# Kernel tuning notes

Measured on AMD Instinct MI355X. Metric: run time of the kernel, lower is better.

The kernel has to match this reference:

```python
import jax, jax.numpy as jnp
import numpy as np

B, H, W, DIM = 64, 28, 28, 384
N = B * H * W
E, K, R = 3, 2, 8
HID = 4 * DIM
SCALING = 8.0 / 8.0  # alpha / r


def setup_inputs() -> dict:
    key = jax.random.key(0)
    ks = jax.random.split(key, 8)
    x = jax.random.normal(ks[0], (B, H, W, DIM), dtype=jnp.float32)
    gate = jax.random.uniform(ks[1], (N, E), dtype=jnp.float32)
    topk_probs = jax.random.uniform(ks[2], (N, K), dtype=jnp.float32)
    topk_idx = jax.random.randint(ks[3], (N, K), 0, E)
    # LoRA expert params (w_up is zeros in the original init; use small randn
    # so the MoE path is numerically non-trivial for kernel testing)
    w_down = jax.random.normal(ks[4], (E, DIM, R), dtype=jnp.float32) * (1.0 / DIM ** 0.5)
    w_up = jax.random.normal(ks[5], (E, R, DIM), dtype=jnp.float32) * 0.02
    # frozen base ConvNeXt MLP: Linear(dim,4dim) -> GELU -> Linear(4dim,dim)
    W1 = jax.random.normal(ks[6], (DIM, HID), dtype=jnp.float32) * 0.02
    b1 = jnp.zeros((HID,), dtype=jnp.float32)
    W2 = jax.random.normal(ks[7], (HID, DIM), dtype=jnp.float32) * 0.02
    b2 = jnp.zeros((DIM,), dtype=jnp.float32)
    return {"x": x, "gate": gate, "topk_probs": topk_probs, "topk_idx": topk_idx,
            "w_down": w_down, "w_up": w_up, "W1": W1, "b1": b1, "W2": W2, "b2": b2}


def reference(x, gate, topk_probs, topk_idx, w_down, w_up, W1, b1, W2, b2):
    gelu = lambda t: jax.nn.gelu(t, approximate=False)  # torch nn.GELU() default = exact erf
    # frozen base MLP
    orig = gelu(jnp.einsum('bhwd,df->bhwf', x, W1) + b1)
    orig = jnp.einsum('bhwf,fd->bhwd', orig, W2) + b2
    # MoE LoRA path over flattened tokens
    x_flat = x.reshape(-1, x.shape[-1])          # [N, dim]
    moe = jnp.zeros_like(x_flat)
    n_experts = w_down.shape[0]
    for i in range(n_experts):
        # combined routing weight for expert i (0 for tokens not routed here)
        prob = jnp.sum(jnp.where(topk_idx == i, topk_probs, 0.0), axis=1)  # [N]
        out_i = gelu(x_flat @ w_down[i]) @ w_up[i] * SCALING               # [N, dim]
        moe = moe + out_i * prob[:, None]
    return orig + moe.reshape(x.shape)
```

## Files before the change

### kernel.cpp

```cpp
#include <hip/hip_runtime.h>
#include <hip/hip_bf16.h>

typedef __attribute__((ext_vector_type(4))) float float4v;
typedef __attribute__((ext_vector_type(8))) __bf16 bf16x8;
typedef __attribute__((ext_vector_type(8))) unsigned short ushort8v;

constexpr int NTOK = 50176;
constexpr int DIM  = 384;
constexpr int HID  = 1536;
constexpr int BM   = 64;
constexpr int NTH  = 512;
constexpr int NBLK = NTOK / BM;
constexpr int CHW  = 32;
constexpr int NCH  = HID / CHW;

constexpr int IMG_WD  = 0;
constexpr int IMG_WUP = 24576;
constexpr int IMG_W1  = 49152;
constexpr int IMG_W2  = 49152 + 48 * 12288 * 2;
constexpr size_t WS_NEED = 2408448;
constexpr int NELEMS = 1204224;

constexpr int L_X  = 0;
constexpr int L_W  = 49152;
constexpr int L_HS = 73728;
constexpr int LDSZ = 81920;

__device__ __forceinline__ unsigned short f2bf(float f) {
  __hip_bfloat16 h = __float2bfloat16(f);
  return *reinterpret_cast<unsigned short*>(&h);
}

__device__ __forceinline__ float gelu_f(float v) {
  float u = 0.7978845608f * (v + 0.044715f * v * v * v);
  float e = __expf(2.0f * u);
  float t = 1.0f - 2.0f / (e + 1.0f);
  return 0.5f * v * (1.0f + t);
}

__device__ __forceinline__ int gt_addr(int r, int s) {
  return ((r >> 3) << 9) + (s << 7) + ((r & 7) << 4);
}

__device__ __forceinline__ void st_load(const char* src, int tid, ushort8v st[3]) {
  #pragma unroll
  for (int j = 0; j < 3; ++j)
    st[j] = *(const ushort8v*)(src + tid * 16 + j * 8192);
}
__device__ __forceinline__ void st_wr(char* dst, int tid, const ushort8v st[3]) {
  #pragma unroll
  for (int j = 0; j < 3; ++j)
    *(ushort8v*)(dst + tid * 16 + j * 8192) = st[j];
}

__global__ __launch_bounds__(256) void pack_k(
    const float* __restrict__ W1, const float* __restrict__ W2,
    const float* __restrict__ wd, const float* __restrict__ wu,
    unsigned short* __restrict__ img)
{
  int i = blockIdx.x * 256 + threadIdx.x;
  if (i >= NELEMS) return;
  if (i < 12288) {
    int f = i / 384; int inb = (i % 384) * 2;
    int d = (inb ^ ((f & 7) << 4)) >> 1;
    float v = (f < 24) ? wd[(f >> 3) * (DIM * 8) + d * 8 + (f & 7)] : 0.f;
    img[i] = f2bf(v);
  } else if (i < 24576) {
    int j = i - 12288;
    int d = j / 32, c = j % 32;
    float v = (c < 24) ? wu[c * DIM + d] : 0.f;
    img[i] = f2bf(v);
  } else if (i < 24576 + 48 * 12288) {
    int j = i - 24576; int h = j / 12288; int jc = j % 12288;
    int f = jc / 384; int inb = (jc % 384) * 2;
    int d = (inb ^ ((f & 7) << 4)) >> 1;
    img[i] = f2bf(W1[d * HID + h * CHW + f]);
  } else {
    int j = i - 24576 - 48 * 12288; int h = j / 12288; int jc = j % 12288;
    int d = jc / 32, k = jc % 32;
    img[i] = f2bf(W2[(h * CHW + k) * DIM + d]);
  }
}

__global__ __launch_bounds__(NTH, 4) void fused_k(
    const float* __restrict__ x,
    const float* __restrict__ tp,
    const int*   __restrict__ ti,
    const float* __restrict__ b1,
    const float* __restrict__ b2,
    const unsigned short* __restrict__ img,
    float* __restrict__ out)
{
  extern __shared__ char lds[];
  const int tid = threadIdx.x, wid = tid >> 6, lane = tid & 63;
  const int lrow = lane & 15, g4 = lane >> 4;
  const int blockRow = blockIdx.x * BM;
  const char* imgc = (const char*)img;

  const int band = wid >> 1, chh = wid & 1;
  const int wr = wid >> 2, wc = wid & 3;

  ushort8v st[3];

  st_load(imgc + IMG_WD, tid, st);
  {
    const float* xb = x + (size_t)blockRow * DIM;
    #pragma unroll
    for (int it = 0; it < 6; ++it) {
      int idx = it * NTH + tid;
      int row = idx / 48, c8 = idx % 48;
      float4v v0 = *(const float4v*)(xb + row * DIM + c8 * 8);
      float4v v1 = *(const float4v*)(xb + row * DIM + c8 * 8 + 4);
      ushort8v u;
      u[0]=f2bf(v0[0]); u[1]=f2bf(v0[1]); u[2]=f2bf(v0[2]); u[3]=f2bf(v0[3]);
      u[4]=f2bf(v1[0]); u[5]=f2bf(v1[1]); u[6]=f2bf(v1[2]); u[7]=f2bf(v1[3]);
      int byte = (row * 768 + c8 * 16) ^ ((row & 7) << 4);
      *(ushort8v*)(lds + L_X + byte) = u;
    }
  }
  st_wr(lds + L_W, tid, st);
  st_load(imgc + IMG_W1, tid, st);
  __syncthreads();

  {
    float4v hv = {};
    int raX = band * 16 + lrow, sA = (raX & 7) << 4, baX = raX * 768 + g4 * 16;
    int rbW = chh * 16 + lrow, sB = (rbW & 7) << 4, baW = rbW * 768 + g4 * 16;
    #pragma unroll
    for (int ks = 0; ks < 12; ++ks) {
      bf16x8 a = *(const bf16x8*)(lds + L_X + ((baX + ks * 64) ^ sA));
      bf16x8 b = *(const bf16x8*)(lds + L_W + ((baW + ks * 64) ^ sB));
      hv = __builtin_amdgcn_mfma_f32_16x16x32_bf16(a, b, hv, 0, 0, 0);
    }
    int colc = chh * 16 + lrow; int e = colc >> 3;
    #pragma unroll
    for (int r = 0; r < 4; ++r) {
      int row = band * 16 + g4 * 4 + r;
      int token = blockRow + row;
      float p = 0.f;
      if (e < 3) {
        int i0 = ti[token * 2], i1 = ti[token * 2 + 1];
        if (i0 == e) p += tp[token * 2];
        if (i1 == e) p += tp[token * 2 + 1];
      }
      float gv = p * gelu_f(hv[r]);
      int byte = gt_addr(row, colc >> 3) + ((colc & 7) << 1);
      *(unsigned short*)(lds + L_HS + byte) = f2bf(gv);
    }
  }
  __syncthreads();
  st_wr(lds + L_W, tid, st);

  float4v acc[2][6] = {};
  {
    bf16x8 bfr[6];
    #pragma unroll
    for (int nt = 0; nt < 6; ++nt) {
      int rd = wc * 96 + nt * 16 + lrow;
      bfr[nt] = *(const bf16x8*)(imgc + IMG_WUP + rd * 64 + g4 * 16);
    }
    bf16x8 A[2];
    #pragma unroll
    for (int mt = 0; mt < 2; ++mt) {
      int ra = wr * 32 + mt * 16 + lrow;
      A[mt] = *(const bf16x8*)(lds + L_HS + gt_addr(ra, g4));
    }
    #pragma unroll
    for (int nt = 0; nt < 6; ++nt) {
      acc[0][nt] = __builtin_amdgcn_mfma_f32_16x16x32_bf16(A[0], bfr[nt], acc[0][nt], 0, 0, 0);
      acc[1][nt] = __builtin_amdgcn_mfma_f32_16x16x32_bf16(A[1], bfr[nt], acc[1][nt], 0, 0, 0);
    }
  }

  for (int h = 0; h < NCH; ++h) {
    const int hb = 4096 - ((h & 1) << 12);
    __syncthreads();
    if (h < NCH - 1)
      st_load(imgc + IMG_W1 + (h + 1) * 24576, tid, st);

    float4v hv = {};
    {
      int raX = band * 16 + lrow, sA = (raX & 7) << 4, baX = raX * 768 + g4 * 16;
      int rbW = chh * 16 + lrow, sB = (rbW & 7) << 4, baW = rbW * 768 + g4 * 16;
      #pragma unroll
      for (int ks = 0; ks < 12; ++ks) {
        bf16x8 a = *(const bf16x8*)(lds + L_X + ((baX + ks * 64) ^ sA));
        bf16x8 b = *(const bf16x8*)(lds + L_W + ((baW + ks * 64) ^ sB));
        hv = __builtin_amdgcn_mfma_f32_16x16x32_bf16(a, b, hv, 0, 0, 0);
      }
    }
    {
      int colc = chh * 16 + lrow;
      float bb = b1[h * CHW + colc];
      #pragma unroll
      for (int r = 0; r < 4; ++r) {
        int row = band * 16 + g4 * 4 + r;
        float gv = gelu_f(hv[r] + bb);
        int byte = gt_addr(row, colc >> 3) + ((colc & 7) << 1);
        *(unsigned short*)(lds + L_HS + hb + byte) = f2bf(gv);
      }
    }
    __syncthreads();
    if (h < NCH - 1)
      st_wr(lds + L_W, tid, st);

    {
      const char* w2b = imgc + IMG_W2 + h * 24576;
      bf16x8 bfr[6];
      #pragma unroll
      for (int nt = 0; nt < 6; ++nt) {
        int rd = wc * 96 + nt * 16 + lrow;
        bfr[nt] = *(const bf16x8*)(w2b + rd * 64 + g4 * 16);
      }
      bf16x8 A[2];
      #pragma unroll
      for (int mt = 0; mt < 2; ++mt) {
        int ra = wr * 32 + mt * 16 + lrow;
        A[mt] = *(const bf16x8*)(lds + L_HS + hb + gt_addr(ra, g4));
      }
      #pragma unroll
      for (int nt = 0; nt < 6; ++nt) {
        acc[0][nt] = __builtin_amdgcn_mfma_f32_16x16x32_bf16(A[0], bfr[nt], acc[0][nt], 0, 0, 0);
        acc[1][nt] = __builtin_amdgcn_mfma_f32_16x16x32_bf16(A[1], bfr[nt], acc[1][nt], 0, 0, 0);
      }
    }
  }

  #pragma unroll
  for (int nt = 0; nt < 6; ++nt) {
    int col = wc * 96 + nt * 16 + lrow;
    float bb = b2[col];
    #pragma unroll
    for (int mt = 0; mt < 2; ++mt) {
      #pragma unroll
      for (int r = 0; r < 4; ++r) {
        int row = wr * 32 + mt * 16 + g4 * 4 + r;
        out[(size_t)(blockRow + row) * DIM + col] = acc[mt][nt][r] + bb;
      }
    }
  }
}

extern "C" void kernel_launch(void* const* d_in, const int* in_sizes, int n_in,
                              void* d_out, int out_size, void* d_ws, size_t ws_size,
                              hipStream_t stream) {
  const float* x          = (const float*)d_in[0];
  const float* topk_probs = (const float*)d_in[2];
  const int*   topk_idx   = (const int*)  d_in[3];
  const float* w_down     = (const float*)d_in[4];
  const float* w_up       = (const float*)d_in[5];
  const float* W1         = (const float*)d_in[6];
  const float* b1         = (const float*)d_in[7];
  const float* W2         = (const float*)d_in[8];
  const float* b2         = (const float*)d_in[9];
  float* out = (float*)d_out;

  if (ws_size < WS_NEED) return;

  hipFuncSetAttribute(reinterpret_cast<const void*>(fused_k),
                      hipFuncAttributeMaxDynamicSharedMemorySize, LDSZ);

  unsigned short* img = (unsigned short*)d_ws;
  pack_k<<<(NELEMS + 255) / 256, 256, 0, stream>>>(W1, W2, w_down, w_up, img);
  fused_k<<<NBLK, NTH, LDSZ, stream>>>(x, topk_probs, topk_idx, b1, b2, img, out);
}
```

Measured before the change: 276.9 us.

## Give each wave its own 16-token strip with register-resident x and double-buffered W1

Reworks the fused MLP kernel so each of 4 waves owns 16 tokens. The bf16 x fragments stay in registers instead of LDS, and each wave computes all 32 hidden columns and all 384 output columns for its strip. W1 chunks are double-buffered in LDS, which removes one barrier per chunk. This cuts LDS traffic and synchronisation, at the cost of a 256-thread block, higher register pressure (24 accumulators plus 12 x fragments) and lower occupancy. Each wave also reads W2 fragments from global memory four times as often per chunk.

```diff
diff --git a/kernel.cpp b/kernel.cpp
--- a/kernel.cpp
+++ b/kernel.cpp
@@ -9,7 +9,7 @@
 constexpr int DIM  = 384;
 constexpr int HID  = 1536;
 constexpr int BM   = 64;
-constexpr int NTH  = 512;
+constexpr int NTH  = 256;
 constexpr int NBLK = NTOK / BM;
 constexpr int CHW  = 32;
 constexpr int NCH  = HID / CHW;
@@ -17,14 +17,12 @@
 constexpr int IMG_WD  = 0;
 constexpr int IMG_WUP = 24576;
 constexpr int IMG_W1  = 49152;
-constexpr int IMG_W2  = 49152 + 48 * 12288 * 2;
+constexpr int IMG_W2  = 49152 + 48 * 24576;
 constexpr size_t WS_NEED = 2408448;
 constexpr int NELEMS = 1204224;
 
-constexpr int L_X  = 0;
-constexpr int L_W  = 49152;
-constexpr int L_HS = 73728;
-constexpr int LDSZ = 81920;
+constexpr int L_HS = 49152;
+constexpr int LDSZ = 53248;
 
 __device__ __forceinline__ unsigned short f2bf(float f) {
   __hip_bfloat16 h = __float2bfloat16(f);
@@ -38,19 +36,26 @@
   return 0.5f * v * (1.0f + t);
 }
 
+__device__ __forceinline__ bf16x8 mk8(float4v a, float4v b) {
+  ushort8v u;
+  u[0]=f2bf(a[0]); u[1]=f2bf(a[1]); u[2]=f2bf(a[2]); u[3]=f2bf(a[3]);
+  u[4]=f2bf(b[0]); u[5]=f2bf(b[1]); u[6]=f2bf(b[2]); u[7]=f2bf(b[3]);
+  return *reinterpret_cast<bf16x8*>(&u);
+}
+
 __device__ __forceinline__ int gt_addr(int r, int s) {
   return ((r >> 3) << 9) + (s << 7) + ((r & 7) << 4);
 }
 
-__device__ __forceinline__ void st_load(const char* src, int tid, ushort8v st[3]) {
+__device__ __forceinline__ void stage_ld(const char* src, int tid, ushort8v t[6]) {
   #pragma unroll
-  for (int j = 0; j < 3; ++j)
-    st[j] = *(const ushort8v*)(src + tid * 16 + j * 8192);
-}
-__device__ __forceinline__ void st_wr(char* dst, int tid, const ushort8v st[3]) {
+  for (int j = 0; j < 6; ++j)
+    t[j] = *(const ushort8v*)(src + tid * 16 + j * 4096);
+}
+__device__ __forceinline__ void stage_wr(char* dst, int tid, const ushort8v t[6]) {
   #pragma unroll
-  for (int j = 0; j < 3; ++j)
-    *(ushort8v*)(dst + tid * 16 + j * 8192) = st[j];
+  for (int j = 0; j < 6; ++j)
+    *(ushort8v*)(dst + tid * 16 + j * 4096) = t[j];
 }
 
 __global__ __launch_bounds__(256) void pack_k(
@@ -82,7 +87,7 @@
   }
 }
 
-__global__ __launch_bounds__(NTH, 4) void fused_k(
+__global__ __launch_bounds__(NTH, 2) void fused_k(
     const float* __restrict__ x,
     const float* __restrict__ tp,
     const int*   __restrict__ ti,
@@ -95,148 +100,108 @@
   const int tid = threadIdx.x, wid = tid >> 6, lane = tid & 63;
   const int lrow = lane & 15, g4 = lane >> 4;
   const int blockRow = blockIdx.x * BM;
+  const int wtok = wid * 16;
   const char* imgc = (const char*)img;
-
-  const int band = wid >> 1, chh = wid & 1;
-  const int wr = wid >> 2, wc = wid & 3;
-
-  ushort8v st[3];
-
-  st_load(imgc + IMG_WD, tid, st);
+  const int swz = (lrow & 7) << 4;
+
+  ushort8v stg[6];
+
+  stage_ld(imgc + IMG_WD, tid, stg);
+  bf16x8 xf[12];
   {
-    const float* xb = x + (size_t)blockRow * DIM;
-    #pragma unroll
-    for (int it = 0; it < 6; ++it) {
-      int idx = it * NTH + tid;
-      int row = idx / 48, c8 = idx % 48;
-      float4v v0 = *(const float4v*)(xb + row * DIM + c8 * 8);
-      float4v v1 = *(const float4v*)(xb + row * DIM + c8 * 8 + 4);
-      ushort8v u;
-      u[0]=f2bf(v0[0]); u[1]=f2bf(v0[1]); u[2]=f2bf(v0[2]); u[3]=f2bf(v0[3]);
-      u[4]=f2bf(v1[0]); u[5]=f2bf(v1[1]); u[6]=f2bf(v1[2]); u[7]=f2bf(v1[3]);
-      int byte = (row * 768 + c8 * 16) ^ ((row & 7) << 4);
-      *(ushort8v*)(lds + L_X + byte) = u;
-    }
-  }
-  st_wr(lds + L_W, tid, st);
-  st_load(imgc + IMG_W1, tid, st);
+    const float* xr = x + (size_t)(blockRow + wtok + lrow) * DIM + g4 * 8;
+    #pragma unroll
+    for (int ks = 0; ks < 12; ++ks) {
+      float4v a = *(const float4v*)(xr + ks * 32);
+      float4v b = *(const float4v*)(xr + ks * 32 + 4);
+      xf[ks] = mk8(a, b);
+    }
+  }
+  stage_wr(lds, tid, stg);
   __syncthreads();
-
+  stage_ld(imgc + IMG_W1, tid, stg);
+
+  float4v acc[24] = {};
   {
-    float4v hv = {};
-    int raX = band * 16 + lrow, sA = (raX & 7) << 4, baX = raX * 768 + g4 * 16;
-    int rbW = chh * 16 + lrow, sB = (rbW & 7) << 4, baW = rbW * 768 + g4 * 16;
+    float4v hv[2] = {};
     #pragma unroll
     for (int ks = 0; ks < 12; ++ks) {
-      bf16x8 a = *(const bf16x8*)(lds + L_X + ((baX + ks * 64) ^ sA));
-      bf16x8 b = *(const bf16x8*)(lds + L_W + ((baW + ks * 64) ^ sB));
-      hv = __builtin_amdgcn_mfma_f32_16x16x32_bf16(a, b, hv, 0, 0, 0);
-    }
-    int colc = chh * 16 + lrow; int e = colc >> 3;
-    #pragma unroll
-    for (int r = 0; r < 4; ++r) {
-      int row = band * 16 + g4 * 4 + r;
-      int token = blockRow + row;
-      float p = 0.f;
-      if (e < 3) {
-        int i0 = ti[token * 2], i1 = ti[token * 2 + 1];
-        if (i0 == e) p += tp[token * 2];
-        if (i1 == e) p += tp[token * 2 + 1];
-      }
-      float gv = p * gelu_f(hv[r]);
-      int byte = gt_addr(row, colc >> 3) + ((colc & 7) << 1);
-      *(unsigned short*)(lds + L_HS + byte) = f2bf(gv);
-    }
-  }
-  __syncthreads();
-  st_wr(lds + L_W, tid, st);
-
-  float4v acc[2][6] = {};
-  {
-    bf16x8 bfr[6];
-    #pragma unroll
-    for (int nt = 0; nt < 6; ++nt) {
-      int rd = wc * 96 + nt * 16 + lrow;
-      bfr[nt] = *(const bf16x8*)(imgc + IMG_WUP + rd * 64 + g4 * 16);
-    }
-    bf16x8 A[2];
-    #pragma unroll
-    for (int mt = 0; mt < 2; ++mt) {
-      int ra = wr * 32 + mt * 16 + lrow;
-      A[mt] = *(const bf16x8*)(lds + L_HS + gt_addr(ra, g4));
-    }
-    #pragma unroll
-    for (int nt = 0; nt < 6; ++nt) {
-      acc[0][nt] = __builtin_amdgcn_mfma_f32_16x16x32_bf16(A[0], bfr[nt], acc[0][nt], 0, 0, 0);
-      acc[1][nt] = __builtin_amdgcn_mfma_f32_16x16x32_bf16(A[1], bfr[nt], acc[1][nt], 0, 0, 0);
-    }
-  }
-
-  for (int h = 0; h < NCH; ++h) {
-    const int hb = 4096 - ((h & 1) << 12);
-    __syncthreads();
-    if (h < NCH - 1)
-      st_load(imgc + IMG_W1 + (h + 1) * 24576, tid, st);
-
-    float4v hv = {};
-    {
-      int raX = band * 16 + lrow, sA = (raX & 7) << 4, baX = raX * 768 + g4 * 16;
-      int rbW = chh * 16 + lrow, sB = (rbW & 7) << 4, baW = rbW * 768 + g4 * 16;
-      #pragma unroll
-      for (int ks = 0; ks < 12; ++ks) {
-        bf16x8 a = *(const bf16x8*)(lds + L_X + ((baX + ks * 64) ^ sA));
-        bf16x8 b = *(const bf16x8*)(lds + L_W + ((baW + ks * 64) ^ sB));
-        hv = __builtin_amdgcn_mfma_f32_16x16x32_bf16(a, b, hv, 0, 0, 0);
-      }
-    }
-    {
-      int colc = chh * 16 + lrow;
-      float bb = b1[h * CHW + colc];
-      #pragma unroll
-      for (int r = 0; r < 4; ++r) {
-        int row = band * 16 + g4 * 4 + r;
-        float gv = gelu_f(hv[r] + bb);
-        int byte = gt_addr(row, colc >> 3) + ((colc & 7) << 1);
-        *(unsigned short*)(lds + L_HS + hb + byte) = f2bf(gv);
-      }
-    }
-    __syncthreads();
-    if (h < NCH - 1)
-      st_wr(lds + L_W, tid, st);
-
-    {
-      const char* w2b = imgc + IMG_W2 + h * 24576;
-      bf16x8 bfr[6];
-      #pragma unroll
-      for (int nt = 0; nt < 6; ++nt) {
-        int rd = wc * 96 + nt * 16 + lrow;
-        bfr[nt] = *(const bf16x8*)(w2b + rd * 64 + g4 * 16);
-      }
-      bf16x8 A[2];
-      #pragma unroll
-      for (int mt = 0; mt < 2; ++mt) {
-        int ra = wr * 32 + mt * 16 + lrow;
-        A[mt] = *(const bf16x8*)(lds + L_HS + hb + gt_addr(ra, g4));
-      }
-      #pragma unroll
-      for (int nt = 0; nt < 6; ++nt) {
-        acc[0][nt] = __builtin_amdgcn_mfma_f32_16x16x32_bf16(A[0], bfr[nt], acc[0][nt], 0, 0, 0);
-        acc[1][nt] = __builtin_amdgcn_mfma_f32_16x16x32_bf16(A[1], bfr[nt], acc[1][nt], 0, 0, 0);
-      }
-    }
-  }
-
-  #pragma unroll
-  for (int nt = 0; nt < 6; ++nt) {
-    int col = wc * 96 + nt * 16 + lrow;
-    float bb = b2[col];
+      bf16x8 b0 = *(const bf16x8*)(lds + (((lrow)      * 768 + ks * 64 + g4 * 16) ^ swz));
+      bf16x8 b1v= *(const bf16x8*)(lds + (((16 + lrow) * 768 + ks * 64 + g4 * 16) ^ swz));
+      hv[0] = __builtin_amdgcn_mfma_f32_16x16x32_bf16(xf[ks], b0,  hv[0], 0, 0, 0);
+      hv[1] = __builtin_amdgcn_mfma_f32_16x16x32_bf16(xf[ks], b1v, hv[1], 0, 0, 0);
+    }
     #pragma unroll
     for (int mt = 0; mt < 2; ++mt) {
       #pragma unroll
       for (int r = 0; r < 4; ++r) {
-        int row = wr * 32 + mt * 16 + g4 * 4 + r;
-        out[(size_t)(blockRow + row) * DIM + col] = acc[mt][nt][r] + bb;
+        int rowl = wtok + g4 * 4 + r;
+        int token = blockRow + rowl;
+        int c = mt * 16 + lrow; int e = c >> 3;
+        float p = 0.f;
+        if (e < 3) {
+          int i0 = ti[token * 2], i1 = ti[token * 2 + 1];
+          if (i0 == e) p += tp[token * 2];
+          if (i1 == e) p += tp[token * 2 + 1];
+        }
+        float gv = p * gelu_f(hv[mt][r]);
+        *(unsigned short*)(lds + L_HS + gt_addr(rowl, c >> 3) + ((c & 7) << 1)) = f2bf(gv);
       }
+    }
+    stage_wr(lds + 24576, tid, stg);
+    bf16x8 ha = *(const bf16x8*)(lds + L_HS + gt_addr(wtok + lrow, g4));
+    #pragma unroll
+    for (int nt = 0; nt < 24; ++nt) {
+      bf16x8 bfr = *(const bf16x8*)(imgc + IMG_WUP + (nt * 16 + lrow) * 64 + g4 * 16);
+      acc[nt] = __builtin_amdgcn_mfma_f32_16x16x32_bf16(ha, bfr, acc[nt], 0, 0, 0);
+    }
+  }
+
+  for (int h = 0; h < NCH; ++h) {
+    __syncthreads();
+    const char* wrd = lds + 24576 * ((h & 1) ^ 1);
+    if (h < NCH - 1)
+      stage_ld(imgc + IMG_W1 + (h + 1) * 24576, tid, stg);
+
+    float4v hv[2] = {};
+    #pragma unroll
+    for (int ks = 0; ks < 12; ++ks) {
+      bf16x8 b0 = *(const bf16x8*)(wrd + (((lrow)      * 768 + ks * 64 + g4 * 16) ^ swz));
+      bf16x8 b1v= *(const bf16x8*)(wrd + (((16 + lrow) * 768 + ks * 64 + g4 * 16) ^ swz));
+      hv[0] = __builtin_amdgcn_mfma_f32_16x16x32_bf16(xf[ks], b0,  hv[0], 0, 0, 0);
+      hv[1] = __builtin_amdgcn_mfma_f32_16x16x32_bf16(xf[ks], b1v, hv[1], 0, 0, 0);
+    }
+    #pragma unroll
+    for (int mt = 0; mt < 2; ++mt) {
+      float bb = b1[h * CHW + mt * 16 + lrow];
+      #pragma unroll
+      for (int r = 0; r < 4; ++r) {
+        int rowl = wtok + g4 * 4 + r;
+        int c = mt * 16 + lrow;
+        float gv = gelu_f(hv[mt][r] + bb);
+        *(unsigned short*)(lds + L_HS + gt_addr(rowl, c >> 3) + ((c & 7) << 1)) = f2bf(gv);
+      }
+    }
+    if (h < NCH - 1)
+      stage_wr(lds + 24576 * (h & 1), tid, stg);
+
+    bf16x8 ha = *(const bf16x8*)(lds + L_HS + gt_addr(wtok + lrow, g4));
+    const char* w2b = imgc + IMG_W2 + h * 24576;
+    #pragma unroll
+    for (int nt = 0; nt < 24; ++nt) {
+      bf16x8 bfr = *(const bf16x8*)(w2b + (nt * 16 + lrow) * 64 + g4 * 16);
+      acc[nt] = __builtin_amdgcn_mfma_f32_16x16x32_bf16(ha, bfr, acc[nt], 0, 0, 0);
+    }
+  }
+
+  #pragma unroll
+  for (int nt = 0; nt < 24; ++nt) {
+    int col = nt * 16 + lrow;
+    float bb = b2[col];
+    #pragma unroll
+    for (int r = 0; r < 4; ++r) {
+      int row = blockRow + wtok + g4 * 4 + r;
+      out[(size_t)row * DIM + col] = acc[nt][r] + bb;
     }
   }
 }
```

Measured after the change: 723.4 us. 161% more time.

## Keep X fragments in registers and double-buffer W1 chunks in LDS

Applied to the files above, without the earlier changes.

The bf16 X tile is loaded once from LDS into per-wave register fragments, so the per-chunk GEMM1 loop reads only W1 from LDS. The freed X region is reused as two W1 chunk buffers that alternate across iterations, and the GELU output buffer becomes single. This cuts LDS traffic and shrinks the LDS footprint from 80KB to 52KB, which may let more blocks fit per CU. In exchange, it adds 48 VGPRs of live X fragments on top of the accumulators, under a launch bound of 4 blocks of 512 threads, which risks register spills.

```diff
diff --git a/kernel.cpp b/kernel.cpp
--- a/kernel.cpp
+++ b/kernel.cpp
@@ -17,14 +17,12 @@
 constexpr int IMG_WD  = 0;
 constexpr int IMG_WUP = 24576;
 constexpr int IMG_W1  = 49152;
-constexpr int IMG_W2  = 49152 + 48 * 12288 * 2;
+constexpr int IMG_W2  = 49152 + 48 * 24576;
 constexpr size_t WS_NEED = 2408448;
 constexpr int NELEMS = 1204224;
 
-constexpr int L_X  = 0;
-constexpr int L_W  = 49152;
-constexpr int L_HS = 73728;
-constexpr int LDSZ = 81920;
+constexpr int L_HS = 49152;
+constexpr int LDSZ = 53248;
 
 __device__ __forceinline__ unsigned short f2bf(float f) {
   __hip_bfloat16 h = __float2bfloat16(f);
@@ -100,9 +98,9 @@
   const int band = wid >> 1, chh = wid & 1;
   const int wr = wid >> 2, wc = wid & 3;
 
-  ushort8v st[3];
-
-  st_load(imgc + IMG_WD, tid, st);
+  ushort8v stg[3];
+
+  st_load(imgc + IMG_WD, tid, stg);
   {
     const float* xb = x + (size_t)blockRow * DIM;
     #pragma unroll
@@ -115,22 +113,33 @@
       u[0]=f2bf(v0[0]); u[1]=f2bf(v0[1]); u[2]=f2bf(v0[2]); u[3]=f2bf(v0[3]);
       u[4]=f2bf(v1[0]); u[5]=f2bf(v1[1]); u[6]=f2bf(v1[2]); u[7]=f2bf(v1[3]);
       int byte = (row * 768 + c8 * 16) ^ ((row & 7) << 4);
-      *(ushort8v*)(lds + L_X + byte) = u;
-    }
-  }
-  st_wr(lds + L_W, tid, st);
-  st_load(imgc + IMG_W1, tid, st);
+      *(ushort8v*)(lds + byte) = u;
+    }
+  }
+  __syncthreads();
+
+  bf16x8 xf[12];
+  {
+    int raX = band * 16 + lrow;
+    int sA = (raX & 7) << 4, baX = raX * 768 + g4 * 16;
+    #pragma unroll
+    for (int ks = 0; ks < 12; ++ks)
+      xf[ks] = *(const bf16x8*)(lds + ((baX + ks * 64) ^ sA));
+  }
+  __syncthreads();
+
+  st_wr(lds, tid, stg);
+  st_load(imgc + IMG_W1, tid, stg);
   __syncthreads();
 
   {
     float4v hv = {};
-    int raX = band * 16 + lrow, sA = (raX & 7) << 4, baX = raX * 768 + g4 * 16;
-    int rbW = chh * 16 + lrow, sB = (rbW & 7) << 4, baW = rbW * 768 + g4 * 16;
+    int rbW = chh * 16 + lrow;
+    int sB = (rbW & 7) << 4, baW = rbW * 768 + g4 * 16;
     #pragma unroll
     for (int ks = 0; ks < 12; ++ks) {
-      bf16x8 a = *(const bf16x8*)(lds + L_X + ((baX + ks * 64) ^ sA));
-      bf16x8 b = *(const bf16x8*)(lds + L_W + ((baW + ks * 64) ^ sB));
-      hv = __builtin_amdgcn_mfma_f32_16x16x32_bf16(a, b, hv, 0, 0, 0);
+      bf16x8 b = *(const bf16x8*)(lds + ((baW + ks * 64) ^ sB));
+      hv = __builtin_amdgcn_mfma_f32_16x16x32_bf16(xf[ks], b, hv, 0, 0, 0);
     }
     int colc = chh * 16 + lrow; int e = colc >> 3;
     #pragma unroll
@@ -144,21 +153,14 @@
         if (i1 == e) p += tp[token * 2 + 1];
       }
       float gv = p * gelu_f(hv[r]);
-      int byte = gt_addr(row, colc >> 3) + ((colc & 7) << 1);
-      *(unsigned short*)(lds + L_HS + byte) = f2bf(gv);
-    }
-  }
-  __syncthreads();
-  st_wr(lds + L_W, tid, st);
+      *(unsigned short*)(lds + L_HS + gt_addr(row, colc >> 3) + ((colc & 7) << 1)) = f2bf(gv);
+    }
+  }
+  __syncthreads();
+  st_wr(lds + 24576, tid, stg);
 
   float4v acc[2][6] = {};
   {
-    bf16x8 bfr[6];
-    #pragma unroll
-    for (int nt = 0; nt < 6; ++nt) {
-      int rd = wc * 96 + nt * 16 + lrow;
-      bfr[nt] = *(const bf16x8*)(imgc + IMG_WUP + rd * 64 + g4 * 16);
-    }
     bf16x8 A[2];
     #pragma unroll
     for (int mt = 0; mt < 2; ++mt) {
@@ -167,26 +169,27 @@
     }
     #pragma unroll
     for (int nt = 0; nt < 6; ++nt) {
-      acc[0][nt] = __builtin_amdgcn_mfma_f32_16x16x32_bf16(A[0], bfr[nt], acc[0][nt], 0, 0, 0);
-      acc[1][nt] = __builtin_amdgcn_mfma_f32_16x16x32_bf16(A[1], bfr[nt], acc[1][nt], 0, 0, 0);
+      int rd = wc * 96 + nt * 16 + lrow;
+      bf16x8 bfr = *(const bf16x8*)(imgc + IMG_WUP + rd * 64 + g4 * 16);
+      acc[0][nt] = __builtin_amdgcn_mfma_f32_16x16x32_bf16(A[0], bfr, acc[0][nt], 0, 0, 0);
+      acc[1][nt] = __builtin_amdgcn_mfma_f32_16x16x32_bf16(A[1], bfr, acc[1][nt], 0, 0, 0);
     }
   }
 
   for (int h = 0; h < NCH; ++h) {
-    const int hb = 4096 - ((h & 1) << 12);
     __syncthreads();
     if (h < NCH - 1)
-      st_load(imgc + IMG_W1 + (h + 1) * 24576, tid, st);
+      st_load(imgc + IMG_W1 + (h + 1) * 24576, tid, stg);
+    const char* bufR = lds + 24576 * ((h + 1) & 1);
 
     float4v hv = {};
     {
-      int raX = band * 16 + lrow, sA = (raX & 7) << 4, baX = raX * 768 + g4 * 16;
-      int rbW = chh * 16 + lrow, sB = (rbW & 7) << 4, baW = rbW * 768 + g4 * 16;
+      int rbW = chh * 16 + lrow;
+      int sB = (rbW & 7) << 4, baW = rbW * 768 + g4 * 16;
       #pragma unroll
       for (int ks = 0; ks < 12; ++ks) {
-        bf16x8 a = *(const bf16x8*)(lds + L_X + ((baX + ks * 64) ^ sA));
-        bf16x8 b = *(const bf16x8*)(lds + L_W + ((baW + ks * 64) ^ sB));
-        hv = __builtin_amdgcn_mfma_f32_16x16x32_bf16(a, b, hv, 0, 0, 0);
+        bf16x8 b = *(const bf16x8*)(bufR + ((baW + ks * 64) ^ sB));
+        hv = __builtin_amdgcn_mfma_f32_16x16x32_bf16(xf[ks], b, hv, 0, 0, 0);
       }
     }
     {
@@ -196,32 +199,27 @@
       for (int r = 0; r < 4; ++r) {
         int row = band * 16 + g4 * 4 + r;
         float gv = gelu_f(hv[r] + bb);
-        int byte = gt_addr(row, colc >> 3) + ((colc & 7) << 1);
-        *(unsigned short*)(lds + L_HS + hb + byte) = f2bf(gv);
+        *(unsigned short*)(lds + L_HS + gt_addr(row, colc >> 3) + ((colc & 7) << 1)) = f2bf(gv);
       }
     }
     __syncthreads();
     if (h < NCH - 1)
-      st_wr(lds + L_W, tid, st);
+      st_wr(lds + 24576 * (h & 1), tid, stg);
 
     {
       const char* w2b = imgc + IMG_W2 + h * 24576;
-      bf16x8 bfr[6];
+      bf16x8 A[2];
+      #pragma unroll
+      for (int mt = 0; mt < 2; ++mt) {
+        int ra = wr * 32 + mt * 16 + lrow;
+        A[mt] = *(const bf16x8*)(lds + L_HS + gt_addr(ra, g4));
+      }
       #pragma unroll
       for (int nt = 0; nt < 6; ++nt) {
         int rd = wc * 96 + nt * 16 + lrow;
-        bfr[nt] = *(const bf16x8*)(w2b + rd * 64 + g4 * 16);
-      }
-      bf16x8 A[2];
-      #pragma unroll
-      for (int mt = 0; mt < 2; ++mt) {
-        int ra = wr * 32 + mt * 16 + lrow;
-        A[mt] = *(const bf16x8*)(lds + L_HS + hb + gt_addr(ra, g4));
-      }
-      #pragma unroll
-      for (int nt = 0; nt < 6; ++nt) {
-        acc[0][nt] = __builtin_amdgcn_mfma_f32_16x16x32_bf16(A[0], bfr[nt], acc[0][nt], 0, 0, 0);
-        acc[1][nt] = __builtin_amdgcn_mfma_f32_16x16x32_bf16(A[1], bfr[nt], acc[1][nt], 0, 0, 0);
+        bf16x8 bfr = *(const bf16x8*)(w2b + rd * 64 + g4 * 16);
+        acc[0][nt] = __builtin_amdgcn_mfma_f32_16x16x32_bf16(A[0], bfr, acc[0][nt], 0, 0, 0);
+        acc[1][nt] = __builtin_amdgcn_mfma_f32_16x16x32_bf16(A[1], bfr, acc[1][nt], 0, 0, 0);
       }
     }
   }
```

Result: slower. 449.6 us (+62.4%).
